# Optimization experiments

Measured on AMD Instinct MI355X. Metric: run time of the kernel, lower is better.

Reference implementation:

```python
import jax, jax.numpy as jnp
import numpy as np

B, T, H = 64, 32, 768          # batch, num query tokens, hidden
E, NB, DFF = 8, 2, 3072        # num_experts, num_beams, expert ffn dim


def setup_inputs() -> dict:
    key = jax.random.key(0)
    ks = jax.random.split(key, 6)
    x = jax.random.normal(ks[0], (B, T, H), dtype=jnp.float32)
    gate_w = jax.random.normal(ks[1], (E, H), dtype=jnp.float32) * 0.02
    w1 = jax.random.normal(ks[2], (E, DFF, H), dtype=jnp.float32) * 0.02
    b1 = jnp.zeros((E, DFF), dtype=jnp.float32)
    w2 = jax.random.normal(ks[3], (E, H, DFF), dtype=jnp.float32) * 0.02
    b2 = jnp.zeros((E, H), dtype=jnp.float32)
    return {"x": x, "gate_w": gate_w, "w1": w1, "b1": b1, "w2": w2, "b2": b2}


def reference(x, gate_w, w1, b1, w2, b2):
    # ---- forward_gate: attention_mask is all ones -> plain mean over tokens ----
    x_avg = jnp.mean(x, axis=1)                         # [B, H]
    logits_gate = x_avg @ gate_w.T                      # [B, E]
    current_scores = jax.nn.softmax(logits_gate, axis=-1)

    # ---- importance auxiliary loss (torch.std is unbiased, ddof=1) ----
    importance = jnp.sum(current_scores, axis=0)        # [E]
    importance_loss = (jnp.std(importance, ddof=1) / jnp.mean(importance)) ** 2

    # ---- beam_search, first layer: exp(log(scores)) == scores; topk num_beams ----
    topk_vals, topk_idx = jax.lax.top_k(current_scores, NB)   # [B, NB]
    beam_scores = topk_vals.reshape(B * NB)
    expert_route = topk_idx.reshape(B * NB, 1).astype(jnp.int32)
    beam_idx = jnp.arange(B * NB, dtype=jnp.int32)

    # ---- replicate x / scores per beam: unsqueeze+expand+view == repeat ----
    x_rep = jnp.repeat(x, NB, axis=0)                   # [B*NB, T, H]
    scores_rep = jnp.repeat(current_scores, NB, axis=0) # [B*NB, E]
    input_x = x_rep[beam_idx]                           # identity gather (faithful)

    # ---- forward_expert_ffn: run ALL experts, then one-hot * prob combine ----
    h = jnp.einsum('bth,efh->betf', input_x, w1) + b1[None, :, None, :]
    h = jax.nn.gelu(h, approximate=False)               # torch nn.GELU default (exact)
    cand = jnp.einsum('betf,ehf->beth', h, w2) + b2[None, :, None, :]  # [B*NB, E, T, H]

    sel = expert_route[:, -1]                           # [B*NB]
    onehot = jax.nn.one_hot(sel, E, dtype=cand.dtype)   # [B*NB, E]
    weights = scores_rep * onehot                       # weight_type == 'ffn_prob'
    output = jnp.einsum('beth,be->bth', cand, weights)  # [B*NB, T, H]

    return output, beam_scores, expert_route, beam_idx, importance_loss
```

## Files before the change

### kernel.cpp

```cpp
#include <hip/hip_runtime.h>
#include <hip/hip_bf16.h>
#include <math.h>

#define Bsz 64
#define T 32
#define H 768
#define E 8
#define NB 2
#define DFF 3072
#define NBEAM (Bsz * NB)
#define NT8MAX 24

#define OUT_BS 3145728
#define OUT_ER 3145856
#define OUT_BI 3145984
#define OUT_IL 3146112

#define WS_LOGITS 0
#define WS_BEAMW  1536
#define WS_SORT   1664
#define WS_T8E    1792
#define WS_T8B    1832
#define WS_T8C    1872
#define WS_XBF    2048
#define WS_HBF    (2048 + 786432)

typedef __attribute__((ext_vector_type(8))) short short8;
typedef __attribute__((ext_vector_type(4))) float f32x4;

__device__ __forceinline__ short8 cvt8(const float4 u, const float4 v) {
    union { short8 s; unsigned w[4]; } r;
    __hip_bfloat162 t;
    t = __float22bfloat162_rn(make_float2(u.x, u.y)); r.w[0] = *(unsigned*)&t;
    t = __float22bfloat162_rn(make_float2(u.z, u.w)); r.w[1] = *(unsigned*)&t;
    t = __float22bfloat162_rn(make_float2(v.x, v.y)); r.w[2] = *(unsigned*)&t;
    t = __float22bfloat162_rn(make_float2(v.z, v.w)); r.w[3] = *(unsigned*)&t;
    return r.s;
}

__device__ __forceinline__ void async16(void* lds, const void* g) {
    __builtin_amdgcn_global_load_lds(
        (const __attribute__((address_space(1))) void*)g,
        (__attribute__((address_space(3))) void*)lds, 16, 0, 0);
}

__global__ __launch_bounds__(256) void gate_conv_kernel(
    const float* __restrict__ x, const float* __restrict__ gate_w,
    ushort* __restrict__ xb, float* __restrict__ logits_part)
{
    __shared__ float part[4][E];
    const int chunk = blockIdx.x, b = blockIdx.y;
    const int tid = threadIdx.x, wv = tid >> 6, lane = tid & 63;
    const int c = chunk * 256 + tid;
    const float* xp = x + (size_t)b * T * H + c;
    ushort* xo = xb + (size_t)b * T * H + c;
    float s = 0.f;
    #pragma unroll
    for (int t = 0; t < T; t += 2) {
        const float f0 = xp[t * H];
        const float f1 = xp[(t + 1) * H];
        s += f0; s += f1;
        __hip_bfloat162 t2 = __float22bfloat162_rn(make_float2(f0, f1));
        const unsigned u = *(const unsigned*)&t2;
        xo[t * H]       = (ushort)(u & 0xffff);
        xo[(t + 1) * H] = (ushort)(u >> 16);
    }
    const float avg = s * (1.0f / T);
    #pragma unroll
    for (int e = 0; e < E; ++e) {
        float p = avg * gate_w[e * H + c];
        #pragma unroll
        for (int off = 32; off; off >>= 1) p += __shfl_down(p, off, 64);
        if (lane == 0) part[wv][e] = p;
    }
    __syncthreads();
    if (tid < E) {
        float t = part[0][tid] + part[1][tid] + part[2][tid] + part[3][tid];
        logits_part[chunk * 512 + b * E + tid] = t;
    }
}

__global__ __launch_bounds__(64) void gating_kernel(
    const float* __restrict__ logits_part, float* __restrict__ beam_w,
    int* __restrict__ sortb, int* __restrict__ t8e, int* __restrict__ t8b,
    int* __restrict__ t8c, float* __restrict__ dout)
{
    const int r = threadIdx.x;
    float v[E];
    float mx = -1e30f;
    #pragma unroll
    for (int e = 0; e < E; ++e) {
        v[e] = logits_part[r * E + e] + logits_part[512 + r * E + e]
             + logits_part[1024 + r * E + e];
        mx = fmaxf(mx, v[e]);
    }
    float s = 0.f;
    #pragma unroll
    for (int e = 0; e < E; ++e) { v[e] = expf(v[e] - mx); s += v[e]; }
    const float inv = 1.0f / s;
    #pragma unroll
    for (int e = 0; e < E; ++e) v[e] *= inv;
    float v0 = -1.f, v1 = -1.f; int i0 = 0, i1 = 0;
    #pragma unroll
    for (int e = 0; e < E; ++e) {
        if (v[e] > v0)      { v1 = v0; i1 = i0; v0 = v[e]; i0 = e; }
        else if (v[e] > v1) { v1 = v[e]; i1 = e; }
    }
    const int b0 = 2 * r, b1 = 2 * r + 1;
    dout[OUT_BS + b0] = v0;          dout[OUT_BS + b1] = v1;
    dout[OUT_ER + b0] = (float)i0;   dout[OUT_ER + b1] = (float)i1;
    dout[OUT_BI + b0] = (float)b0;   dout[OUT_BI + b1] = (float)b1;
    beam_w[b0] = v0;  beam_w[b1] = v1;
    float imp[E];
    #pragma unroll
    for (int e = 0; e < E; ++e) {
        float t = v[e];
        #pragma unroll
        for (int off = 1; off < 64; off <<= 1) t += __shfl_xor(t, off, 64);
        imp[e] = t;
    }
    if (r == 0) {
        float tot = 0.f;
        #pragma unroll
        for (int e = 0; e < E; ++e) tot += imp[e];
        const float mean = tot / E;
        float var = 0.f;
        #pragma unroll
        for (int e = 0; e < E; ++e) { float d = imp[e] - mean; var += d * d; }
        var /= (E - 1);
        dout[OUT_IL] = var / (mean * mean);
    }
    unsigned long long m0[E], m1[E];
    #pragma unroll
    for (int e = 0; e < E; ++e) {
        m0[e] = __ballot(i0 == e);
        m1[e] = __ballot(i1 == e);
    }
    int cnt[E], off[E];
    int a0 = 0;
    #pragma unroll
    for (int e = 0; e < E; ++e) {
        cnt[e] = __popcll(m0[e]) + __popcll(m1[e]);
        off[e] = a0; a0 += cnt[e];
    }
    const unsigned long long below = (r == 0) ? 0ull : ((1ull << r) - 1ull);
    const unsigned long long incl  = below | (1ull << r);
    const int pos0 = __popcll(m0[i0] & below) + __popcll(m1[i0] & below);
    const int pos1 = __popcll(m0[i1] & incl)  + __popcll(m1[i1] & below);
    sortb[off[i0] + pos0] = b0;
    sortb[off[i1] + pos1] = b1;
    if (r == 0) {
        int tiles[E];
        int used[NT8MAX];
        for (int t = 0; t < NT8MAX; ++t) used[t] = 0;
        #pragma unroll
        for (int e = 0; e < E; ++e) tiles[e] = (cnt[e] + 7) >> 3;
        #pragma unroll
        for (int e = 0; e < E; ++e) {
            const int k = tiles[e] < 3 ? tiles[e] : 3;
            for (int i = 0; i < k; ++i) {
                const int sl = 3 * e + i;
                t8e[sl] = e; t8b[sl] = off[e] + 8 * i;
                const int rem = cnt[e] - 8 * i;
                t8c[sl] = rem < 8 ? rem : 8;
                used[sl] = 1;
            }
        }
        int fs[NT8MAX]; int nf = 0;
        for (int round = 0; round < 3; ++round)
            for (int c = 0; c < E; ++c) {
                const int sl = 3 * c + round;
                if (!used[sl]) fs[nf++] = sl;
            }
        int fp = 0;
        for (int e = 0; e < E; ++e)
            for (int i = 3; i < tiles[e]; ++i) {
                const int sl = fs[fp++];
                t8e[sl] = e; t8b[sl] = off[e] + 8 * i;
                const int rem = cnt[e] - 8 * i;
                t8c[sl] = rem < 8 ? rem : 8;
                used[sl] = 1;
            }
        for (int t = 0; t < NT8MAX; ++t) if (!used[t]) t8c[t] = 0;
    }
}

template <int KTOT, int NTILE, bool DO_GELU, int NSLICE>
__global__ __launch_bounds__(256, 2) void moe_ffn_mfma(
    const ushort* __restrict__ Abf, int a_div,
    const float* __restrict__ Wf32, int w_rows,
    const float* __restrict__ biasb,
    const int* __restrict__ sortb, const int* __restrict__ t8e,
    const int* __restrict__ t8b, const int* __restrict__ t8c,
    const float* __restrict__ beam_w,
    void* __restrict__ Obase)
{
    constexpr int KSPAN = KTOT / NSLICE;
    constexpr int KT    = KSPAN / 32;
    constexpr int NFRAG = NTILE / 32;
    constexpr int WSLOT = NTILE / 64;
    __shared__ __align__(16) ushort sA[2][256 * 32];
    __shared__ __align__(16) ushort sB[2][NTILE * 32];

    const int nx  = gridDim.x;
    const int nwg = nx * gridDim.y;
    const int hw  = blockIdx.y * nx + blockIdx.x;
    const int q8  = nwg >> 3;
    const int lid = (hw & 7) * q8 + (hw >> 3);
    const int tile  = lid % NT8MAX;
    const int rr    = lid / NT8MAX;
    const int strip = rr % nx;
    const int k0    = (rr / nx) * KSPAN;

    const int cnt  = t8c[tile];
    if (cnt == 0) return;
    const int e    = t8e[tile];
    const int base = t8b[tile];
    const int tid  = threadIdx.x;
    const int wv   = tid >> 6;
    const int lane = tid & 63;
    const int quad = lane >> 4;
    const int l16  = lane & 15;
    const int mh   = (wv & 1) * 128;
    const int nh   = (wv >> 1) * (NTILE / 2);
    const int n0   = strip * NTILE;

    int bm[8];
    #pragma unroll
    for (int s = 0; s < 8; ++s) bm[s] = sortb[base + (s < cnt ? s : cnt - 1)];

    const ushort* aseg[4];
    #pragma unroll
    for (int jj = 0; jj < 4; ++jj) {
        const int s = (wv * 4 + jj) * 64 + lane;
        const int r = s >> 2;
        const int c = (s & 3) ^ ((s >> 3) & 3);
        aseg[jj] = Abf + (size_t)(bm[r >> 5] / a_div) * T * KTOT
                 + (size_t)(r & 31) * KTOT + c * 8 + k0;
    }
    const float* wseg[WSLOT];
    int wslot[WSLOT];
    #pragma unroll
    for (int jj = 0; jj < WSLOT; ++jj) {
        const int s = jj * 256 + tid;
        const int r = s >> 2;
        const int c = (s & 3) ^ ((s >> 3) & 3);
        wseg[jj] = Wf32 + (size_t)e * w_rows * KTOT + (size_t)(n0 + r) * KTOT
                 + c * 8 + k0;
        wslot[jj] = s * 8;
    }

    const int fx = (l16 >> 1) & 3;
    int aoff[8], boff[NFRAG];
    #pragma unroll
    for (int mt = 0; mt < 8; ++mt)
        aoff[mt] = (mh + mt * 16 + l16) * 32 + ((quad ^ fx) * 8);
    #pragma unroll
    for (int nt = 0; nt < NFRAG; ++nt)
        boff[nt] = (nh + nt * 16 + l16) * 32 + ((quad ^ fx) * 8);

    float4 wr[WSLOT][2];
    #pragma unroll
    for (int jj = 0; jj < WSLOT; ++jj) {
        wr[jj][0] = *(const float4*)(wseg[jj]);
        wr[jj][1] = *(const float4*)(wseg[jj] + 4);
    }
    #pragma unroll
    for (int jj = 0; jj < 4; ++jj)
        async16((char*)sA[0] + (wv * 4 + jj) * 1024, aseg[jj]);

    f32x4 acc[8][NFRAG];
    #pragma unroll
    for (int mt = 0; mt < 8; ++mt)
        #pragma unroll
        for (int nt = 0; nt < NFRAG; ++nt) acc[mt][nt] = {0.f, 0.f, 0.f, 0.f};

    for (int kt = 0; kt < KT; ++kt) {
        const int p = kt & 1;
        #pragma unroll
        for (int jj = 0; jj < WSLOT; ++jj)
            *(short8*)(sB[p] + wslot[jj]) = cvt8(wr[jj][0], wr[jj][1]);
        __syncthreads();
        if (kt + 1 < KT) {
            const int kn = (kt + 1) * 32;
            #pragma unroll
            for (int jj = 0; jj < 4; ++jj)
                async16((char*)sA[1 - p] + (wv * 4 + jj) * 1024, aseg[jj] + kn);
            #pragma unroll
            for (int jj = 0; jj < WSLOT; ++jj) {
                wr[jj][0] = *(const float4*)(wseg[jj] + kn);
                wr[jj][1] = *(const float4*)(wseg[jj] + kn + 4);
            }
        }
        short8 wf[NFRAG];
        #pragma unroll
        for (int nt = 0; nt < NFRAG; ++nt)
            wf[nt] = *(const short8*)(sB[p] + boff[nt]);
        #pragma unroll
        for (int mt = 0; mt < 8; ++mt) {
            const short8 af = *(const short8*)(sA[p] + aoff[mt]);
            #pragma unroll
            for (int nt = 0; nt < NFRAG; ++nt)
                acc[mt][nt] = __builtin_amdgcn_mfma_f32_16x16x32_bf16(
                    af, wf[nt], acc[mt][nt], 0, 0, 0);
        }
    }

    #pragma unroll
    for (int nt = 0; nt < NFRAG; ++nt) {
        const int n = n0 + nh + nt * 16 + l16;
        const float bias = biasb[(size_t)e * w_rows + n];
        #pragma unroll
        for (int mt = 0; mt < 8; ++mt) {
            const int rowb = mh + mt * 16 + quad * 4;
            const int s = rowb >> 5;
            if (s >= cnt) continue;
            const int b = bm[s];
            const float scale = DO_GELU ? 1.0f : beam_w[b];
            #pragma unroll
            for (int r = 0; r < 4; ++r) {
                const int t = (rowb + r) & 31;
                const size_t idx = (size_t)b * T * w_rows + (size_t)t * w_rows + n;
                if (DO_GELU) {
                    float vv = acc[mt][nt][r] + bias;
                    vv = 0.5f * vv * (1.0f + erff(vv * 0.70710678118654752f));
                    ((__hip_bfloat16*)Obase)[idx] = __float2bfloat16(vv);
                } else {
                    float vv = acc[mt][nt][r] + ((k0 == 0) ? bias : 0.f);
                    atomicAdd((float*)Obase + idx, vv * scale);
                }
            }
        }
    }
}

extern "C" void kernel_launch(void* const* d_in, const int* in_sizes, int n_in,
                              void* d_out, int out_size, void* d_ws, size_t ws_size,
                              hipStream_t stream)
{
    const float* x      = (const float*)d_in[0];
    const float* gate_w = (const float*)d_in[1];
    const float* w1     = (const float*)d_in[2];
    const float* b1     = (const float*)d_in[3];
    const float* w2     = (const float*)d_in[4];
    const float* b2     = (const float*)d_in[5];
    float* out = (float*)d_out;
    float* ws  = (float*)d_ws;

    float*  logits = ws + WS_LOGITS;
    float*  beam_w = ws + WS_BEAMW;
    int*    sortb  = (int*)(ws + WS_SORT);
    int*    t8e    = (int*)(ws + WS_T8E);
    int*    t8b    = (int*)(ws + WS_T8B);
    int*    t8c    = (int*)(ws + WS_T8C);
    ushort* x_bf   = (ushort*)(ws + WS_XBF);
    ushort* h_bf   = (ushort*)(ws + WS_HBF);

    hipMemsetAsync(out, 0, (size_t)NBEAM * T * H * sizeof(float), stream);

    gate_conv_kernel<<<dim3(3, Bsz), 256, 0, stream>>>(x, gate_w, x_bf, logits);
    gating_kernel<<<1, 64, 0, stream>>>(logits, beam_w, sortb, t8e, t8b, t8c, out);
    moe_ffn_mfma<H, 128, true, 1><<<dim3(DFF / 128, NT8MAX), 256, 0, stream>>>(
        x_bf, NB, w1, DFF, b1, sortb, t8e, t8b, t8c, beam_w, (void*)h_bf);
    moe_ffn_mfma<DFF, 128, false, 4><<<dim3(H / 128, NT8MAX * 4), 256, 0, stream>>>(
        h_bf, 1, w2, H, b2, sortb, t8e, t8b, t8c, beam_w, out);
}
```

Before: 316.4 us.

## Deepen MoE FFN GEMM pipeline to three LDS stages with explicit waitcnts

Replaces the double-buffered K loop with a three-stage pipeline. A tiles arrive via async copies and W tiles go through rotating register sets, prefetched two k-steps ahead. It uses hand-placed s_waitcnt vmcnt/lgkmcnt and a raw s_barrier in place of __syncthreads, aiming to hide global-load latency behind the MFMA work. The cost is more LDS (which may cut occupancy at 2 blocks per CU), more registers, and the requirement that KT be divisible by 3. The hardcoded vmcnt count is fragile if the number of loads per stage changes.

```diff
diff --git a/kernel.cpp b/kernel.cpp
--- a/kernel.cpp
+++ b/kernel.cpp
@@ -197,10 +197,11 @@
 {
     constexpr int KSPAN = KTOT / NSLICE;
     constexpr int KT    = KSPAN / 32;
+    static_assert(KT % 3 == 0, "3-stage pipeline needs KT % 3 == 0");
     constexpr int NFRAG = NTILE / 32;
     constexpr int WSLOT = NTILE / 64;
-    __shared__ __align__(16) ushort sA[2][256 * 32];
-    __shared__ __align__(16) ushort sB[2][NTILE * 32];
+    __shared__ __align__(16) ushort sA[3][256 * 32];
+    __shared__ __align__(16) ushort sB[3][NTILE * 32];
 
     const int nx  = gridDim.x;
     const int nwg = nx * gridDim.y;
@@ -259,51 +260,73 @@
     for (int nt = 0; nt < NFRAG; ++nt)
         boff[nt] = (nh + nt * 16 + l16) * 32 + ((quad ^ fx) * 8);
 
-    float4 wr[WSLOT][2];
+    f32x4 acc[8][NFRAG];
+    #pragma unroll
+    for (int mt = 0; mt < 8; ++mt)
+        #pragma unroll
+        for (int nt = 0; nt < NFRAG; ++nt) acc[mt][nt] = {0.f, 0.f, 0.f, 0.f};
+
+    float4 wrA[WSLOT][2], wrB[WSLOT][2], wrC[WSLOT][2];
+
+    #pragma unroll
+    for (int jj = 0; jj < 4; ++jj)
+        async16((char*)&sA[0][0] + (wv * 4 + jj) * 1024, aseg[jj]);
     #pragma unroll
     for (int jj = 0; jj < WSLOT; ++jj) {
-        wr[jj][0] = *(const float4*)(wseg[jj]);
-        wr[jj][1] = *(const float4*)(wseg[jj] + 4);
-    }
+        wrA[jj][0] = *(const float4*)(wseg[jj]);
+        wrA[jj][1] = *(const float4*)(wseg[jj] + 4);
+    }
+    asm volatile("" ::: "memory");
     #pragma unroll
     for (int jj = 0; jj < 4; ++jj)
-        async16((char*)sA[0] + (wv * 4 + jj) * 1024, aseg[jj]);
-
-    f32x4 acc[8][NFRAG];
-    #pragma unroll
-    for (int mt = 0; mt < 8; ++mt)
-        #pragma unroll
-        for (int nt = 0; nt < NFRAG; ++nt) acc[mt][nt] = {0.f, 0.f, 0.f, 0.f};
-
-    for (int kt = 0; kt < KT; ++kt) {
-        const int p = kt & 1;
+        async16((char*)&sA[1][0] + (wv * 4 + jj) * 1024, aseg[jj] + 32);
+    #pragma unroll
+    for (int jj = 0; jj < WSLOT; ++jj) {
+        wrB[jj][0] = *(const float4*)(wseg[jj] + 32);
+        wrB[jj][1] = *(const float4*)(wseg[jj] + 32 + 4);
+    }
+
+    auto body = [&](int kt, int stage, float4 (&wcur)[WSLOT][2],
+                    float4 (&wnxt)[WSLOT][2]) {
+        if (kt + 1 < KT) asm volatile("s_waitcnt vmcnt(8)" ::: "memory");
+        else             asm volatile("s_waitcnt vmcnt(0)" ::: "memory");
+        __builtin_amdgcn_sched_barrier(0);
         #pragma unroll
         for (int jj = 0; jj < WSLOT; ++jj)
-            *(short8*)(sB[p] + wslot[jj]) = cvt8(wr[jj][0], wr[jj][1]);
-        __syncthreads();
-        if (kt + 1 < KT) {
-            const int kn = (kt + 1) * 32;
+            *(short8*)(&sB[stage][0] + wslot[jj]) = cvt8(wcur[jj][0], wcur[jj][1]);
+        asm volatile("s_waitcnt lgkmcnt(0)" ::: "memory");
+        __builtin_amdgcn_s_barrier();
+        if (kt + 2 < KT) {
+            const int kn = (kt + 2) * 32;
+            const int nstage = (stage + 2 >= 3) ? (stage - 1) : (stage + 2);
             #pragma unroll
             for (int jj = 0; jj < 4; ++jj)
-                async16((char*)sA[1 - p] + (wv * 4 + jj) * 1024, aseg[jj] + kn);
+                async16((char*)&sA[nstage][0] + (wv * 4 + jj) * 1024,
+                        aseg[jj] + kn);
             #pragma unroll
             for (int jj = 0; jj < WSLOT; ++jj) {
-                wr[jj][0] = *(const float4*)(wseg[jj] + kn);
-                wr[jj][1] = *(const float4*)(wseg[jj] + kn + 4);
+                wnxt[jj][0] = *(const float4*)(wseg[jj] + kn);
+                wnxt[jj][1] = *(const float4*)(wseg[jj] + kn + 4);
             }
         }
         short8 wf[NFRAG];
         #pragma unroll
         for (int nt = 0; nt < NFRAG; ++nt)
-            wf[nt] = *(const short8*)(sB[p] + boff[nt]);
+            wf[nt] = *(const short8*)(&sB[stage][0] + boff[nt]);
         #pragma unroll
         for (int mt = 0; mt < 8; ++mt) {
-            const short8 af = *(const short8*)(sA[p] + aoff[mt]);
+            const short8 af = *(const short8*)(&sA[stage][0] + aoff[mt]);
             #pragma unroll
             for (int nt = 0; nt < NFRAG; ++nt)
                 acc[mt][nt] = __builtin_amdgcn_mfma_f32_16x16x32_bf16(
                     af, wf[nt], acc[mt][nt], 0, 0, 0);
         }
+    };
+
+    for (int kt = 0; kt < KT; kt += 3) {
+        body(kt + 0, 0, wrA, wrC);
+        body(kt + 1, 1, wrB, wrA);
+        body(kt + 2, 2, wrC, wrB);
     }
 
     #pragma unroll
```

New measurement: 330.5 us. 1.04x slower.

## Pre-stage expert weights into swizzled bf16 tiles for async LDS loading

Applied to the files above, without the earlier changes.

Adds a kernel that converts the fp32 expert weights into bf16, laid out as 128x32 swizzled tiles. A new GEMM kernel then streams those tiles straight into LDS with async global-to-LDS loads instead of converting fp32 in registers. Which path runs depends on workspace size: both weight sets staged, only w2 staged, or the original direct path. The conversion runs on every call, which adds a full read of the fp32 weights and a bf16 write. The hope is that cheaper, better-pipelined weight loads in the GEMMs outweigh that extra traffic.

```diff
diff --git a/kernel.cpp b/kernel.cpp
--- a/kernel.cpp
+++ b/kernel.cpp
@@ -24,6 +24,10 @@
 #define WS_T8C    1872
 #define WS_XBF    2048
 #define WS_HBF    (2048 + 786432)
+#define WS_W1S    (WS_HBF + 6291456)
+#define WS_W2S    (WS_W1S + 9437184)
+#define WS_NEED_ONE  ((size_t)(WS_W1S + 9437184) * 4)
+#define WS_NEED_BOTH ((size_t)(WS_W2S + 9437184) * 4)
 
 typedef __attribute__((ext_vector_type(8))) short short8;
 typedef __attribute__((ext_vector_type(4))) float f32x4;
@@ -42,6 +46,29 @@
     __builtin_amdgcn_global_load_lds(
         (const __attribute__((address_space(1))) void*)g,
         (__attribute__((address_space(3))) void*)lds, 16, 0, 0);
+}
+
+__global__ __launch_bounds__(256) void stage_w_kernel(
+    const float* __restrict__ src, ushort* __restrict__ dst,
+    int R, int K)
+{
+    const int kc8 = K >> 3;
+    const int chunk = blockIdx.x * 256 + threadIdx.x;
+    const int g    = chunk / kc8;
+    const int kidx = chunk - g * kc8;
+    const int e    = g / R;
+    const int row  = g - e * R;
+    const float4 u = *(const float4*)(src + (size_t)chunk * 8);
+    const float4 v = *(const float4*)(src + (size_t)chunk * 8 + 4);
+    const short8 val = cvt8(u, v);
+    const int kt    = kidx >> 2;
+    const int pos   = kidx & 3;
+    const int strip = row >> 7;
+    const int rloc  = row & 127;
+    const int p     = pos ^ ((rloc >> 1) & 3);
+    const int s     = (rloc << 2) | p;
+    const size_t tb = ((((size_t)e * (R >> 7) + strip) * (K >> 5)) + kt) * 4096;
+    *(short8*)(dst + tb + s * 8) = val;
 }
 
 __global__ __launch_bounds__(256) void gate_conv_kernel(
@@ -185,8 +212,146 @@
     }
 }
 
+template <int KTOT, int RTOT, bool DO_GELU, int NSLICE>
+__global__ __launch_bounds__(256, 2) void moe_ffn_staged(
+    const ushort* __restrict__ Abf, int a_div,
+    const ushort* __restrict__ Wst,
+    const float* __restrict__ biasb,
+    const int* __restrict__ sortb, const int* __restrict__ t8e,
+    const int* __restrict__ t8b, const int* __restrict__ t8c,
+    const float* __restrict__ beam_w,
+    void* __restrict__ Obase)
+{
+    constexpr int KSPAN = KTOT / NSLICE;
+    constexpr int KT    = KSPAN / 32;
+    constexpr int NFRAG = 4;
+    __shared__ __align__(16) ushort sA[2][256 * 32];
+    __shared__ __align__(16) ushort sB[2][128 * 32];
+
+    const int nx  = gridDim.x;
+    const int nwg = nx * gridDim.y;
+    const int hw  = blockIdx.y * nx + blockIdx.x;
+    const int q8  = nwg >> 3;
+    const int lid = (hw & 7) * q8 + (hw >> 3);
+    const int tile  = lid % NT8MAX;
+    const int rr    = lid / NT8MAX;
+    const int strip = rr % nx;
+    const int k0    = (rr / nx) * KSPAN;
+
+    const int cnt  = t8c[tile];
+    if (cnt == 0) return;
+    const int e    = t8e[tile];
+    const int base = t8b[tile];
+    const int tid  = threadIdx.x;
+    const int wv   = tid >> 6;
+    const int lane = tid & 63;
+    const int quad = lane >> 4;
+    const int l16  = lane & 15;
+    const int mh   = (wv & 1) * 128;
+    const int nh   = (wv >> 1) * 64;
+    const int n0   = strip * 128;
+
+    int bm[8];
+    #pragma unroll
+    for (int s = 0; s < 8; ++s) bm[s] = sortb[base + (s < cnt ? s : cnt - 1)];
+
+    const ushort* aseg[4];
+    #pragma unroll
+    for (int jj = 0; jj < 4; ++jj) {
+        const int s = (wv * 4 + jj) * 64 + lane;
+        const int r = s >> 2;
+        const int c = (s & 3) ^ ((s >> 3) & 3);
+        aseg[jj] = Abf + (size_t)(bm[r >> 5] / a_div) * T * KTOT
+                 + (size_t)(r & 31) * KTOT + c * 8 + k0;
+    }
+    const ushort* wseg[2];
+    {
+        const ushort* wtile0 = Wst
+            + ((((size_t)e * (RTOT >> 7) + strip) * (KTOT >> 5)) + (k0 >> 5)) * 4096;
+        #pragma unroll
+        for (int jj = 0; jj < 2; ++jj)
+            wseg[jj] = wtile0 + ((wv * 2 + jj) * 64 + lane) * 8;
+    }
+
+    const int fx = (l16 >> 1) & 3;
+    int aoff[8], boff[NFRAG];
+    #pragma unroll
+    for (int mt = 0; mt < 8; ++mt)
+        aoff[mt] = (mh + mt * 16 + l16) * 32 + ((quad ^ fx) * 8);
+    #pragma unroll
+    for (int nt = 0; nt < NFRAG; ++nt)
+        boff[nt] = (nh + nt * 16 + l16) * 32 + ((quad ^ fx) * 8);
+
+    #pragma unroll
+    for (int jj = 0; jj < 4; ++jj)
+        async16((char*)sA[0] + (wv * 4 + jj) * 1024, aseg[jj]);
+    #pragma unroll
+    for (int jj = 0; jj < 2; ++jj)
+        async16((char*)sB[0] + (wv * 2 + jj) * 1024, wseg[jj]);
+
+    f32x4 acc[8][NFRAG];
+    #pragma unroll
+    for (int mt = 0; mt < 8; ++mt)
+        #pragma unroll
+        for (int nt = 0; nt < NFRAG; ++nt) acc[mt][nt] = {0.f, 0.f, 0.f, 0.f};
+
+    for (int kt = 0; kt < KT; ++kt) {
+        const int p = kt & 1;
+        __syncthreads();
+        if (kt + 1 < KT) {
+            #pragma unroll
+            for (int jj = 0; jj < 4; ++jj)
+                async16((char*)sA[1 - p] + (wv * 4 + jj) * 1024,
+                        aseg[jj] + (kt + 1) * 32);
+            #pragma unroll
+            for (int jj = 0; jj < 2; ++jj)
+                async16((char*)sB[1 - p] + (wv * 2 + jj) * 1024,
+                        wseg[jj] + (size_t)(kt + 1) * 4096);
+        }
+        short8 wf[NFRAG];
+        #pragma unroll
+        for (int nt = 0; nt < NFRAG; ++nt)
+            wf[nt] = *(const short8*)(sB[p] + boff[nt]);
+        #pragma unroll
+        for (int mt = 0; mt < 8; ++mt) {
+            const short8 af = *(const short8*)(sA[p] + aoff[mt]);
+            #pragma unroll
+            for (int nt = 0; nt < NFRAG; ++nt)
+                acc[mt][nt] = __builtin_amdgcn_mfma_f32_16x16x32_bf16(
+                    af, wf[nt], acc[mt][nt], 0, 0, 0);
+        }
+    }
+
+    #pragma unroll
+    for (int nt = 0; nt < NFRAG; ++nt) {
+        const int n = n0 + nh + nt * 16 + l16;
+        const float bias = biasb[(size_t)e * RTOT + n];
+        #pragma unroll
+        for (int mt = 0; mt < 8; ++mt) {
+            const int rowb = mh + mt * 16 + quad * 4;
+            const int s = rowb >> 5;
+            if (s >= cnt) continue;
+            const int b = bm[s];
+            const float scale = DO_GELU ? 1.0f : beam_w[b];
+            #pragma unroll
+            for (int r = 0; r < 4; ++r) {
+                const int t = (rowb + r) & 31;
+                const size_t idx = (size_t)b * T * RTOT + (size_t)t * RTOT + n;
+                if (DO_GELU) {
+                    float vv = acc[mt][nt][r] + bias;
+                    vv = 0.5f * vv * (1.0f + erff(vv * 0.70710678118654752f));
+                    ((__hip_bfloat16*)Obase)[idx] = __float2bfloat16(vv);
+                } else {
+                    float vv = acc[mt][nt][r] + ((k0 == 0) ? bias : 0.f);
+                    atomicAdd((float*)Obase + idx, vv * scale);
+                }
+            }
+        }
+    }
+}
+
 template <int KTOT, int NTILE, bool DO_GELU, int NSLICE>
-__global__ __launch_bounds__(256, 2) void moe_ffn_mfma(
+__global__ __launch_bounds__(256, 2) void moe_ffn_direct(
     const ushort* __restrict__ Abf, int a_div,
     const float* __restrict__ Wf32, int w_rows,
     const float* __restrict__ biasb,
@@ -355,13 +520,35 @@
     int*    t8c    = (int*)(ws + WS_T8C);
     ushort* x_bf   = (ushort*)(ws + WS_XBF);
     ushort* h_bf   = (ushort*)(ws + WS_HBF);
+    ushort* w1s    = (ushort*)(ws + WS_W1S);
+    ushort* w2s    = (ushort*)(ws + WS_W2S);
 
     hipMemsetAsync(out, 0, (size_t)NBEAM * T * H * sizeof(float), stream);
 
+    const int mode = (ws_size >= WS_NEED_BOTH) ? 2
+                   : (ws_size >= WS_NEED_ONE)  ? 1 : 0;
+    if (mode == 2) {
+        stage_w_kernel<<<9216, 256, 0, stream>>>(w1, w1s, DFF, H);
+        stage_w_kernel<<<9216, 256, 0, stream>>>(w2, w2s, H, DFF);
+    } else if (mode == 1) {
+        stage_w_kernel<<<9216, 256, 0, stream>>>(w2, w1s, H, DFF);
+    }
     gate_conv_kernel<<<dim3(3, Bsz), 256, 0, stream>>>(x, gate_w, x_bf, logits);
     gating_kernel<<<1, 64, 0, stream>>>(logits, beam_w, sortb, t8e, t8b, t8c, out);
-    moe_ffn_mfma<H, 128, true, 1><<<dim3(DFF / 128, NT8MAX), 256, 0, stream>>>(
-        x_bf, NB, w1, DFF, b1, sortb, t8e, t8b, t8c, beam_w, (void*)h_bf);
-    moe_ffn_mfma<DFF, 128, false, 4><<<dim3(H / 128, NT8MAX * 4), 256, 0, stream>>>(
-        h_bf, 1, w2, H, b2, sortb, t8e, t8b, t8c, beam_w, out);
-}
+
+    if (mode == 2)
+        moe_ffn_staged<H, DFF, true, 1><<<dim3(DFF / 128, NT8MAX), 256, 0, stream>>>(
+            x_bf, NB, w1s, b1, sortb, t8e, t8b, t8c, beam_w, (void*)h_bf);
+    else
+        moe_ffn_direct<H, 128, true, 1><<<dim3(DFF / 128, NT8MAX), 256, 0, stream>>>(
+            x_bf, NB, w1, DFF, b1, sortb, t8e, t8b, t8c, beam_w, (void*)h_bf);
+
+    if (mode >= 1) {
+        const ushort* w2stage = (mode == 2) ? w2s : w1s;
+        moe_ffn_staged<DFF, H, false, 4><<<dim3(H / 128, NT8MAX * 4), 256, 0, stream>>>(
+            h_bf, 1, w2stage, b2, sortb, t8e, t8b, t8c, beam_w, out);
+    } else {
+        moe_ffn_direct<DFF, 128, false, 4><<<dim3(H / 128, NT8MAX * 4), 256, 0, stream>>>(
+            h_bf, 1, w2, H, b2, sortb, t8e, t8b, t8c, beam_w, out);
+    }
+}
```

Result: slower. 369.3 us (+16.7%).

## Fuse all MoE stages into one cooperative persistent kernel with grid syncs

Applied to the files above, without the earlier changes.

Replaces the memset plus four separate launches with a single cooperative kernel of 576 blocks. Grid-wide syncs separate the zeroing/gate-conversion, gating, FFN1 and FFN2 phases, and every block recomputes the routing into shared memory. The aim is to remove launch gaps and the single-block gating kernel on the critical path. The cost is requiring 576 blocks co-resident (3 per CU) and paying grid.sync overhead; if the cooperative launch fails, the old multi-kernel path runs instead.

```diff
diff --git a/kernel.cpp b/kernel.cpp
--- a/kernel.cpp
+++ b/kernel.cpp
@@ -1,6 +1,9 @@
 #include <hip/hip_runtime.h>
 #include <hip/hip_bf16.h>
+#include <hip/hip_cooperative_groups.h>
 #include <math.h>
+
+namespace cg = cooperative_groups;
 
 #define Bsz 64
 #define T 32
@@ -10,6 +13,7 @@
 #define DFF 3072
 #define NBEAM (Bsz * NB)
 #define NT8MAX 24
+#define NBLK 576
 
 #define OUT_BS 3145728
 #define OUT_ER 3145856
@@ -42,6 +46,324 @@
     __builtin_amdgcn_global_load_lds(
         (const __attribute__((address_space(1))) void*)g,
         (__attribute__((address_space(3))) void*)lds, 16, 0, 0);
+}
+
+template <int KTOT, bool DO_GELU, int NSLICE, int NX>
+__device__ __forceinline__ void gemm_body(
+    int hw,
+    const ushort* __restrict__ Abf, int a_div,
+    const float* __restrict__ Wf32, int w_rows,
+    const float* __restrict__ biasb,
+    const int* sortb, const int* t8e, const int* t8b, const int* t8c,
+    const float* beamw, void* __restrict__ Obase,
+    ushort (*sA)[256 * 32], ushort (*sB)[128 * 32])
+{
+    constexpr int KSPAN = KTOT / NSLICE;
+    constexpr int KT    = KSPAN / 32;
+    constexpr int NFRAG = 4;
+    constexpr int WSLOT = 2;
+
+    const int q8  = NBLK >> 3;
+    const int lid = (hw & 7) * q8 + (hw >> 3);
+    const int tile  = lid % NT8MAX;
+    const int rr    = lid / NT8MAX;
+    const int strip = rr % NX;
+    const int k0    = (rr / NX) * KSPAN;
+
+    const int cnt  = t8c[tile];
+    if (cnt == 0) return;
+    const int e    = t8e[tile];
+    const int base = t8b[tile];
+    const int tid  = threadIdx.x;
+    const int wv   = tid >> 6;
+    const int lane = tid & 63;
+    const int quad = lane >> 4;
+    const int l16  = lane & 15;
+    const int mh   = (wv & 1) * 128;
+    const int nh   = (wv >> 1) * 64;
+    const int n0   = strip * 128;
+
+    int bm[8];
+    #pragma unroll
+    for (int s = 0; s < 8; ++s) bm[s] = sortb[base + (s < cnt ? s : cnt - 1)];
+
+    const ushort* aseg[4];
+    #pragma unroll
+    for (int jj = 0; jj < 4; ++jj) {
+        const int s = (wv * 4 + jj) * 64 + lane;
+        const int r = s >> 2;
+        const int c = (s & 3) ^ ((s >> 3) & 3);
+        aseg[jj] = Abf + (size_t)(bm[r >> 5] / a_div) * T * KTOT
+                 + (size_t)(r & 31) * KTOT + c * 8 + k0;
+    }
+    const float* wseg[WSLOT];
+    int wslot[WSLOT];
+    #pragma unroll
+    for (int jj = 0; jj < WSLOT; ++jj) {
+        const int s = jj * 256 + tid;
+        const int r = s >> 2;
+        const int c = (s & 3) ^ ((s >> 3) & 3);
+        wseg[jj] = Wf32 + (size_t)e * w_rows * KTOT + (size_t)(n0 + r) * KTOT
+                 + c * 8 + k0;
+        wslot[jj] = s * 8;
+    }
+
+    const int fx = (l16 >> 1) & 3;
+    int aoff[8], boff[NFRAG];
+    #pragma unroll
+    for (int mt = 0; mt < 8; ++mt)
+        aoff[mt] = (mh + mt * 16 + l16) * 32 + ((quad ^ fx) * 8);
+    #pragma unroll
+    for (int nt = 0; nt < NFRAG; ++nt)
+        boff[nt] = (nh + nt * 16 + l16) * 32 + ((quad ^ fx) * 8);
+
+    float4 wr[WSLOT][2];
+    #pragma unroll
+    for (int jj = 0; jj < WSLOT; ++jj) {
+        wr[jj][0] = *(const float4*)(wseg[jj]);
+        wr[jj][1] = *(const float4*)(wseg[jj] + 4);
+    }
+    #pragma unroll
+    for (int jj = 0; jj < 4; ++jj)
+        async16((char*)sA[0] + (wv * 4 + jj) * 1024, aseg[jj]);
+
+    f32x4 acc[8][NFRAG];
+    #pragma unroll
+    for (int mt = 0; mt < 8; ++mt)
+        #pragma unroll
+        for (int nt = 0; nt < NFRAG; ++nt) acc[mt][nt] = {0.f, 0.f, 0.f, 0.f};
+
+    for (int kt = 0; kt < KT; ++kt) {
+        const int p = kt & 1;
+        #pragma unroll
+        for (int jj = 0; jj < WSLOT; ++jj)
+            *(short8*)(sB[p] + wslot[jj]) = cvt8(wr[jj][0], wr[jj][1]);
+        __syncthreads();
+        if (kt + 1 < KT) {
+            const int kn = (kt + 1) * 32;
+            #pragma unroll
+            for (int jj = 0; jj < 4; ++jj)
+                async16((char*)sA[1 - p] + (wv * 4 + jj) * 1024, aseg[jj] + kn);
+            #pragma unroll
+            for (int jj = 0; jj < WSLOT; ++jj) {
+                wr[jj][0] = *(const float4*)(wseg[jj] + kn);
+                wr[jj][1] = *(const float4*)(wseg[jj] + kn + 4);
+            }
+        }
+        short8 wf[NFRAG];
+        #pragma unroll
+        for (int nt = 0; nt < NFRAG; ++nt)
+            wf[nt] = *(const short8*)(sB[p] + boff[nt]);
+        #pragma unroll
+        for (int mt = 0; mt < 8; ++mt) {
+            const short8 af = *(const short8*)(sA[p] + aoff[mt]);
+            #pragma unroll
+            for (int nt = 0; nt < NFRAG; ++nt)
+                acc[mt][nt] = __builtin_amdgcn_mfma_f32_16x16x32_bf16(
+                    af, wf[nt], acc[mt][nt], 0, 0, 0);
+        }
+    }
+    __syncthreads();
+
+    #pragma unroll
+    for (int nt = 0; nt < NFRAG; ++nt) {
+        const int n = n0 + nh + nt * 16 + l16;
+        const float bias = biasb[(size_t)e * w_rows + n];
+        #pragma unroll
+        for (int mt = 0; mt < 8; ++mt) {
+            const int rowb = mh + mt * 16 + quad * 4;
+            const int s = rowb >> 5;
+            if (s >= cnt) continue;
+            const int b = bm[s];
+            const float scale = DO_GELU ? 1.0f : beamw[b];
+            #pragma unroll
+            for (int r = 0; r < 4; ++r) {
+                const int t = (rowb + r) & 31;
+                const size_t idx = (size_t)b * T * w_rows + (size_t)t * w_rows + n;
+                if (DO_GELU) {
+                    float vv = acc[mt][nt][r] + bias;
+                    vv = 0.5f * vv * (1.0f + erff(vv * 0.70710678118654752f));
+                    ((__hip_bfloat16*)Obase)[idx] = __float2bfloat16(vv);
+                } else {
+                    float vv = acc[mt][nt][r] + ((k0 == 0) ? bias : 0.f);
+                    atomicAdd((float*)Obase + idx, vv * scale);
+                }
+            }
+        }
+    }
+}
+
+__global__ __launch_bounds__(256, 3) void fused_moe(
+    const float* __restrict__ x, const float* __restrict__ gate_w,
+    const float* __restrict__ w1, const float* __restrict__ b1,
+    const float* __restrict__ w2, const float* __restrict__ b2,
+    float* __restrict__ out, ushort* __restrict__ x_bf,
+    ushort* __restrict__ h_bf, float* __restrict__ logits)
+{
+    __shared__ __align__(16) ushort sA[2][256 * 32];
+    __shared__ __align__(16) ushort sB[2][128 * 32];
+    __shared__ float ls_part[4][E];
+    __shared__ float ls_beamw[NBEAM];
+    __shared__ int   ls_sortb[NBEAM];
+    __shared__ int   ls_t8e[NT8MAX], ls_t8b[NT8MAX], ls_t8c[NT8MAX];
+
+    const int hw  = blockIdx.x;
+    const int tid = threadIdx.x;
+    cg::grid_group grid = cg::this_grid();
+
+    {
+        float4 z = {0.f, 0.f, 0.f, 0.f};
+        for (int i = hw * 256 + tid; i < (NBEAM * T * H / 4); i += NBLK * 256)
+            ((float4*)out)[i] = z;
+    }
+    if (hw < 192) {
+        const int chunk = hw % 3, b = hw / 3;
+        const int wv = tid >> 6, lane = tid & 63;
+        const int c = chunk * 256 + tid;
+        const float* xp = x + (size_t)b * T * H + c;
+        ushort* xo = x_bf + (size_t)b * T * H + c;
+        float s = 0.f;
+        #pragma unroll
+        for (int t = 0; t < T; t += 2) {
+            const float f0 = xp[t * H];
+            const float f1 = xp[(t + 1) * H];
+            s += f0; s += f1;
+            __hip_bfloat162 t2 = __float22bfloat162_rn(make_float2(f0, f1));
+            const unsigned u = *(const unsigned*)&t2;
+            xo[t * H]       = (ushort)(u & 0xffff);
+            xo[(t + 1) * H] = (ushort)(u >> 16);
+        }
+        const float avg = s * (1.0f / T);
+        #pragma unroll
+        for (int e = 0; e < E; ++e) {
+            float p = avg * gate_w[e * H + c];
+            #pragma unroll
+            for (int off = 32; off; off >>= 1) p += __shfl_down(p, off, 64);
+            if (lane == 0) ls_part[wv][e] = p;
+        }
+        __syncthreads();
+        if (tid < E) {
+            float t = ls_part[0][tid] + ls_part[1][tid]
+                    + ls_part[2][tid] + ls_part[3][tid];
+            logits[chunk * 512 + b * E + tid] = t;
+        }
+    }
+
+    grid.sync();
+
+    if (tid < 64) {
+        const int r = tid;
+        float v[E];
+        float mx = -1e30f;
+        #pragma unroll
+        for (int e = 0; e < E; ++e) {
+            v[e] = logits[r * E + e] + logits[512 + r * E + e]
+                 + logits[1024 + r * E + e];
+            mx = fmaxf(mx, v[e]);
+        }
+        float s = 0.f;
+        #pragma unroll
+        for (int e = 0; e < E; ++e) { v[e] = expf(v[e] - mx); s += v[e]; }
+        const float inv = 1.0f / s;
+        #pragma unroll
+        for (int e = 0; e < E; ++e) v[e] *= inv;
+        float v0 = -1.f, v1 = -1.f; int i0 = 0, i1 = 0;
+        #pragma unroll
+        for (int e = 0; e < E; ++e) {
+            if (v[e] > v0)      { v1 = v0; i1 = i0; v0 = v[e]; i0 = e; }
+            else if (v[e] > v1) { v1 = v[e]; i1 = e; }
+        }
+        const int b0 = 2 * r, b1 = 2 * r + 1;
+        ls_beamw[b0] = v0;  ls_beamw[b1] = v1;
+        if (hw == 0) {
+            out[OUT_BS + b0] = v0;          out[OUT_BS + b1] = v1;
+            out[OUT_ER + b0] = (float)i0;   out[OUT_ER + b1] = (float)i1;
+            out[OUT_BI + b0] = (float)b0;   out[OUT_BI + b1] = (float)b1;
+            float imp[E];
+            #pragma unroll
+            for (int e = 0; e < E; ++e) {
+                float t = v[e];
+                #pragma unroll
+                for (int off = 1; off < 64; off <<= 1) t += __shfl_xor(t, off, 64);
+                imp[e] = t;
+            }
+            if (r == 0) {
+                float tot = 0.f;
+                #pragma unroll
+                for (int e = 0; e < E; ++e) tot += imp[e];
+                const float mean = tot / E;
+                float var = 0.f;
+                #pragma unroll
+                for (int e = 0; e < E; ++e) { float d = imp[e] - mean; var += d * d; }
+                var /= (E - 1);
+                out[OUT_IL] = var / (mean * mean);
+            }
+        }
+        unsigned long long m0[E], m1[E];
+        #pragma unroll
+        for (int e = 0; e < E; ++e) {
+            m0[e] = __ballot(i0 == e);
+            m1[e] = __ballot(i1 == e);
+        }
+        int cnt[E], off[E];
+        int a0 = 0;
+        #pragma unroll
+        for (int e = 0; e < E; ++e) {
+            cnt[e] = __popcll(m0[e]) + __popcll(m1[e]);
+            off[e] = a0; a0 += cnt[e];
+        }
+        const unsigned long long below = (r == 0) ? 0ull : ((1ull << r) - 1ull);
+        const unsigned long long incl  = below | (1ull << r);
+        const int pos0 = __popcll(m0[i0] & below) + __popcll(m1[i0] & below);
+        const int pos1 = __popcll(m0[i1] & incl)  + __popcll(m1[i1] & below);
+        ls_sortb[off[i0] + pos0] = b0;
+        ls_sortb[off[i1] + pos1] = b1;
+        if (r == 0) {
+            int tiles[E];
+            int used[NT8MAX];
+            for (int t = 0; t < NT8MAX; ++t) used[t] = 0;
+            #pragma unroll
+            for (int e = 0; e < E; ++e) tiles[e] = (cnt[e] + 7) >> 3;
+            #pragma unroll
+            for (int e = 0; e < E; ++e) {
+                const int k = tiles[e] < 3 ? tiles[e] : 3;
+                for (int i = 0; i < k; ++i) {
+                    const int sl = 3 * e + i;
+                    ls_t8e[sl] = e; ls_t8b[sl] = off[e] + 8 * i;
+                    const int rem = cnt[e] - 8 * i;
+                    ls_t8c[sl] = rem < 8 ? rem : 8;
+                    used[sl] = 1;
+                }
+            }
+            int fs[NT8MAX]; int nf = 0;
+            for (int round = 0; round < 3; ++round)
+                for (int c = 0; c < E; ++c) {
+                    const int sl = 3 * c + round;
+                    if (!used[sl]) fs[nf++] = sl;
+                }
+            int fp = 0;
+            for (int e = 0; e < E; ++e)
+                for (int i = 3; i < tiles[e]; ++i) {
+                    const int sl = fs[fp++];
+                    ls_t8e[sl] = e; ls_t8b[sl] = off[e] + 8 * i;
+                    const int rem = cnt[e] - 8 * i;
+                    ls_t8c[sl] = rem < 8 ? rem : 8;
+                    used[sl] = 1;
+                }
+            for (int t = 0; t < NT8MAX; ++t) if (!used[t]) ls_t8c[t] = 0;
+        }
+    }
+    __syncthreads();
+
+    gemm_body<H, true, 1, 24>(hw, x_bf, NB, w1, DFF, b1,
+                              ls_sortb, ls_t8e, ls_t8b, ls_t8c, ls_beamw,
+                              (void*)h_bf, sA, sB);
+
+    grid.sync();
+
+    gemm_body<DFF, false, 4, 6>(hw, h_bf, 1, w2, H, b2,
+                                ls_sortb, ls_t8e, ls_t8b, ls_t8c, ls_beamw,
+                                (void*)out, sA, sB);
 }
 
 __global__ __launch_bounds__(256) void gate_conv_kernel(
@@ -185,8 +507,8 @@
     }
 }
 
-template <int KTOT, int NTILE, bool DO_GELU, int NSLICE>
-__global__ __launch_bounds__(256, 2) void moe_ffn_mfma(
+template <int KTOT, bool DO_GELU, int NSLICE, int NX>
+__global__ __launch_bounds__(256, 2) void moe_ffn_direct(
     const ushort* __restrict__ Abf, int a_div,
     const float* __restrict__ Wf32, int w_rows,
     const float* __restrict__ biasb,
@@ -195,143 +517,12 @@
     const float* __restrict__ beam_w,
     void* __restrict__ Obase)
 {
-    constexpr int KSPAN = KTOT / NSLICE;
-    constexpr int KT    = KSPAN / 32;
-    constexpr int NFRAG = NTILE / 32;
-    constexpr int WSLOT = NTILE / 64;
     __shared__ __align__(16) ushort sA[2][256 * 32];
-    __shared__ __align__(16) ushort sB[2][NTILE * 32];
-
-    const int nx  = gridDim.x;
-    const int nwg = nx * gridDim.y;
-    const int hw  = blockIdx.y * nx + blockIdx.x;
-    const int q8  = nwg >> 3;
-    const int lid = (hw & 7) * q8 + (hw >> 3);
-    const int tile  = lid % NT8MAX;
-    const int rr    = lid / NT8MAX;
-    const int strip = rr % nx;
-    const int k0    = (rr / nx) * KSPAN;
-
-    const int cnt  = t8c[tile];
-    if (cnt == 0) return;
-    const int e    = t8e[tile];
-    const int base = t8b[tile];
-    const int tid  = threadIdx.x;
-    const int wv   = tid >> 6;
-    const int lane = tid & 63;
-    const int quad = lane >> 4;
-    const int l16  = lane & 15;
-    const int mh   = (wv & 1) * 128;
-    const int nh   = (wv >> 1) * (NTILE / 2);
-    const int n0   = strip * NTILE;
-
-    int bm[8];
-    #pragma unroll
-    for (int s = 0; s < 8; ++s) bm[s] = sortb[base + (s < cnt ? s : cnt - 1)];
-
-    const ushort* aseg[4];
-    #pragma unroll
-    for (int jj = 0; jj < 4; ++jj) {
-        const int s = (wv * 4 + jj) * 64 + lane;
-        const int r = s >> 2;
-        const int c = (s & 3) ^ ((s >> 3) & 3);
-        aseg[jj] = Abf + (size_t)(bm[r >> 5] / a_div) * T * KTOT
-                 + (size_t)(r & 31) * KTOT + c * 8 + k0;
-    }
-    const float* wseg[WSLOT];
-    int wslot[WSLOT];
-    #pragma unroll
-    for (int jj = 0; jj < WSLOT; ++jj) {
-        const int s = jj * 256 + tid;
-        const int r = s >> 2;
-        const int c = (s & 3) ^ ((s >> 3) & 3);
-        wseg[jj] = Wf32 + (size_t)e * w_rows * KTOT + (size_t)(n0 + r) * KTOT
-                 + c * 8 + k0;
-        wslot[jj] = s * 8;
-    }
-
-    const int fx = (l16 >> 1) & 3;
-    int aoff[8], boff[NFRAG];
-    #pragma unroll
-    for (int mt = 0; mt < 8; ++mt)
-        aoff[mt] = (mh + mt * 16 + l16) * 32 + ((quad ^ fx) * 8);
-    #pragma unroll
-    for (int nt = 0; nt < NFRAG; ++nt)
-        boff[nt] = (nh + nt * 16 + l16) * 32 + ((quad ^ fx) * 8);
-
-    float4 wr[WSLOT][2];
-    #pragma unroll
-    for (int jj = 0; jj < WSLOT; ++jj) {
-        wr[jj][0] = *(const float4*)(wseg[jj]);
-        wr[jj][1] = *(const float4*)(wseg[jj] + 4);
-    }
-    #pragma unroll
-    for (int jj = 0; jj < 4; ++jj)
-        async16((char*)sA[0] + (wv * 4 + jj) * 1024, aseg[jj]);
-
-    f32x4 acc[8][NFRAG];
-    #pragma unroll
-    for (int mt = 0; mt < 8; ++mt)
-        #pragma unroll
-        for (int nt = 0; nt < NFRAG; ++nt) acc[mt][nt] = {0.f, 0.f, 0.f, 0.f};
-
-    for (int kt = 0; kt < KT; ++kt) {
-        const int p = kt & 1;
-        #pragma unroll
-        for (int jj = 0; jj < WSLOT; ++jj)
-            *(short8*)(sB[p] + wslot[jj]) = cvt8(wr[jj][0], wr[jj][1]);
-        __syncthreads();
-        if (kt + 1 < KT) {
-            const int kn = (kt + 1) * 32;
-            #pragma unroll
-            for (int jj = 0; jj < 4; ++jj)
-                async16((char*)sA[1 - p] + (wv * 4 + jj) * 1024, aseg[jj] + kn);
-            #pragma unroll
-            for (int jj = 0; jj < WSLOT; ++jj) {
-                wr[jj][0] = *(const float4*)(wseg[jj] + kn);
-                wr[jj][1] = *(const float4*)(wseg[jj] + kn + 4);
-            }
-        }
-        short8 wf[NFRAG];
-        #pragma unroll
-        for (int nt = 0; nt < NFRAG; ++nt)
-            wf[nt] = *(const short8*)(sB[p] + boff[nt]);
-        #pragma unroll
-        for (int mt = 0; mt < 8; ++mt) {
-            const short8 af = *(const short8*)(sA[p] + aoff[mt]);
-            #pragma unroll
-            for (int nt = 0; nt < NFRAG; ++nt)
-                acc[mt][nt] = __builtin_amdgcn_mfma_f32_16x16x32_bf16(
-                    af, wf[nt], acc[mt][nt], 0, 0, 0);
-        }
-    }
-
-    #pragma unroll
-    for (int nt = 0; nt < NFRAG; ++nt) {
-        const int n = n0 + nh + nt * 16 + l16;
-        const float bias = biasb[(size_t)e * w_rows + n];
-        #pragma unroll
-        for (int mt = 0; mt < 8; ++mt) {
-            const int rowb = mh + mt * 16 + quad * 4;
-            const int s = rowb >> 5;
-            if (s >= cnt) continue;
-            const int b = bm[s];
-            const float scale = DO_GELU ? 1.0f : beam_w[b];
-            #pragma unroll
-            for (int r = 0; r < 4; ++r) {
-                const int t = (rowb + r) & 31;
-                const size_t idx = (size_t)b * T * w_rows + (size_t)t * w_rows + n;
-                if (DO_GELU) {
-                    float vv = acc[mt][nt][r] + bias;
-                    vv = 0.5f * vv * (1.0f + erff(vv * 0.70710678118654752f));
-                    ((__hip_bfloat16*)Obase)[idx] = __float2bfloat16(vv);
-                } else {
-                    float vv = acc[mt][nt][r] + ((k0 == 0) ? bias : 0.f);
-                    atomicAdd((float*)Obase + idx, vv * scale);
-                }
-            }
-        }
-    }
+    __shared__ __align__(16) ushort sB[2][128 * 32];
+    const int hw = blockIdx.y * gridDim.x + blockIdx.x;
+    gemm_body<KTOT, DO_GELU, NSLICE, NX>(hw, Abf, a_div, Wf32, w_rows, biasb,
+                                         sortb, t8e, t8b, t8c, beam_w, Obase,
+                                         sA, sB);
 }
 
 extern "C" void kernel_launch(void* const* d_in, const int* in_sizes, int n_in,
@@ -356,12 +547,19 @@
     ushort* x_bf   = (ushort*)(ws + WS_XBF);
     ushort* h_bf   = (ushort*)(ws + WS_HBF);
 
+    void* kargs[] = {
+        (void*)&x, (void*)&gate_w, (void*)&w1, (void*)&b1, (void*)&w2,
+        (void*)&b2, (void*)&out, (void*)&x_bf, (void*)&h_bf, (void*)&logits
+    };
+    hipError_t err = hipLaunchCooperativeKernel(
+        (const void*)fused_moe, dim3(NBLK), dim3(256), kargs, 0, stream);
+    if (err == hipSuccess) return;
+
     hipMemsetAsync(out, 0, (size_t)NBEAM * T * H * sizeof(float), stream);
-
     gate_conv_kernel<<<dim3(3, Bsz), 256, 0, stream>>>(x, gate_w, x_bf, logits);
     gating_kernel<<<1, 64, 0, stream>>>(logits, beam_w, sortb, t8e, t8b, t8c, out);
-    moe_ffn_mfma<H, 128, true, 1><<<dim3(DFF / 128, NT8MAX), 256, 0, stream>>>(
+    moe_ffn_direct<H, true, 1, 24><<<dim3(24, 24), 256, 0, stream>>>(
         x_bf, NB, w1, DFF, b1, sortb, t8e, t8b, t8c, beam_w, (void*)h_bf);
-    moe_ffn_mfma<DFF, 128, false, 4><<<dim3(H / 128, NT8MAX * 4), 256, 0, stream>>>(
+    moe_ffn_direct<DFF, false, 4, 6><<<dim3(6, 96), 256, 0, stream>>>(
         h_bf, 1, w2, H, b2, sortb, t8e, t8b, t8c, beam_w, out);
 }
```

New measurement: 461.5 us. +45.9%, slower.
